# Kernel tuning notes

Measured on AMD Instinct MI355X. Metric: run time of the kernel, lower is better.

The kernel has to match this reference:

```python
import jax, jax.numpy as jnp
import numpy as np

B, CIN, COUT, H, W, DC = 16, 256, 256, 64, 64, 3


def _i2s_mask():
    # MaskedConv2d type 'B', 1x1 kernel: keep (out,in) where in-group <= out-group (mod data_channels)
    oc = np.arange(COUT) % DC
    ic = np.arange(CIN) % DC
    return jnp.asarray((ic[None, :] <= oc[:, None]).astype(np.float32))


def setup_inputs() -> dict:
    key = jax.random.key(0)
    ks = jax.random.split(key, 9)
    s = 0.05
    return {
        "x": jax.random.normal(ks[0], (B, CIN, H, W), jnp.float32),
        "w_i2s": jax.random.normal(ks[1], (COUT, CIN), jnp.float32) * s,
        "b_i2s": jax.random.normal(ks[2], (COUT,), jnp.float32) * s,
        "w_ih": jax.random.normal(ks[3], (4 * COUT, COUT), jnp.float32) * s,
        "b_ih": jax.random.normal(ks[4], (4 * COUT,), jnp.float32) * s,
        "b_hh": jax.random.normal(ks[5], (4 * COUT,), jnp.float32) * s,
        "k0": jax.random.normal(ks[6], (COUT, COUT), jnp.float32) * s,
        "k1": jax.random.normal(ks[7], (COUT, COUT), jnp.float32) * s,
        "b_s2s": jax.random.normal(ks[8], (COUT,), jnp.float32) * s,
    }


def _shift(x):
    # skew: row i shifted right by i -> [b, c, h, 2w-1]
    b, c, h, w = x.shape
    rows = jnp.arange(h)[:, None]
    cols = rows + jnp.arange(w)[None, :]
    out = jnp.zeros((b, c, h, 2 * w - 1), x.dtype)
    return out.at[:, :, rows, cols].set(x)


def _unshift(x, w):
    h = x.shape[2]
    rows = jnp.arange(h)[:, None]
    cols = rows + jnp.arange(w)[None, :]
    return x[:, :, rows, cols]  # [b, c, h, w]


def _diag_lstm(x, w_i2s, b_i2s, w_ih, b_ih, b_hh, k0, k1, b_s2s):
    b, _, h, w = x.shape
    wd = 2 * w - 1
    # masked 1x1 input-to-state conv on the skewed map
    xs = jnp.einsum('oc,bchw->bohw', w_i2s * _i2s_mask(), _shift(x)) + b_i2s[None, :, None, None]
    # per-step inputs: [wd, b*h, cout], rows flattened in (batch, height) order
    xs = xs.transpose(3, 0, 2, 1).reshape(wd, b * h, COUT)
    bias = b_ih + b_hh  # h0 is zeroed every step in the original, so W_hh never contributes

    def step(carry, x_t):
        h_prev, c = carry
        # state-to-state Conv2d k=(2,1), padding='same' (right-pad only) along flattened b*h axis
        h_next = jnp.concatenate([h_prev[1:], jnp.zeros((1, COUT), x_t.dtype)], axis=0)
        s2s = h_prev @ k0.T + h_next @ k1.T + b_s2s
        gates = (x_t + s2s) @ w_ih.T + bias
        i, f, g, o = jnp.split(gates, 4, axis=-1)
        c = jax.nn.sigmoid(f) * c + jax.nn.sigmoid(i) * jnp.tanh(g)
        h_new = jax.nn.sigmoid(o) * jnp.tanh(c)
        return (h_new, c), h_new

    z = jnp.zeros((b * h, COUT), x.dtype)
    _, hs = jax.lax.scan(step, (z, z), xs)
    # faithful to original raw .view(b, cout, h, 1): plain reshape, NOT a transpose
    outs = hs.reshape(wd, b, COUT, h).transpose(1, 2, 3, 0)  # [b, cout, h, wd]
    return _unshift(outs, w)


def reference(x, w_i2s, b_i2s, w_ih, b_ih, b_hh, k0, k1, b_s2s):
    params = (w_i2s, b_i2s, w_ih, b_ih, b_hh, k0, k1, b_s2s)
    left = _diag_lstm(x, *params)
    right = jnp.flip(_diag_lstm(jnp.flip(x, 3), *params), 3)
    right = jnp.concatenate(
        [jnp.zeros_like(right[:, :, :1, :]), right[:, :, :-1, :]], axis=2)
    return left + right
```

## Files before the change

kernel.cpp:

```cpp
#include <hip/hip_runtime.h>
#include <cstdint>
#include <cstddef>

#define BB_ 16
#define HH_ 64
#define WW_ 64
#define CC_ 256
#define WD_ 127
#define RPD 1024
#define RT_ 2048
#define NBLK 256

typedef float  f32x4 __attribute__((ext_vector_type(4)));
typedef short  s16x8 __attribute__((ext_vector_type(8)));
typedef int    i32x4 __attribute__((ext_vector_type(4)));

__device__ __forceinline__ unsigned short f2bf(float f) {
  unsigned u = __float_as_uint(f);
  u += 0x7fffu + ((u >> 16) & 1u);
  return (unsigned short)(u >> 16);
}
__device__ __forceinline__ float bf2f(unsigned short h) {
  return __uint_as_float(((unsigned)h) << 16);
}

__global__ __launch_bounds__(256) void prep_kernel(
    const float* __restrict__ w_i2s, const float* __restrict__ b_i2s,
    const float* __restrict__ w_ih,  const float* __restrict__ b_ih,
    const float* __restrict__ b_hh,  const float* __restrict__ b_s2s,
    float* __restrict__ wm, unsigned short* __restrict__ XP,
    float* __restrict__ cvec, float* __restrict__ gbias,
    unsigned* __restrict__ cnt) {
  int idx = blockIdx.x * 256 + threadIdx.x;
  if (idx < 65536) {
    int c = idx >> 8, ci = idx & 255;
    wm[idx] = ((ci % 3) <= (c % 3)) ? w_i2s[idx] : 0.0f;
  }
  int i3 = idx - 65536;
  if (i3 >= 0 && i3 < 262144) {
    int n = i3 >> 8, k = i3 & 255;
    int chb = n >> 6, g = (n >> 4) & 3, cl = n & 15;
    int j = g * 256 + chb * 16 + cl;
    float val = w_ih[j * 256 + k];
    int ks = k >> 5, l4k = (k >> 3) & 3, e = k & 7;
    size_t o = (size_t)chb * 16384 + (size_t)(ks * 4 + g) * 512 +
               (size_t)(l4k * 16 + cl) * 8 + e;
    XP[o] = f2bf(val);
  }
  int i4 = idx - 327680;
  if (i4 >= 0 && i4 < 256) cvec[i4] = b_i2s[i4] + b_s2s[i4];
  int i5 = idx - 327936;
  if (i5 >= 0 && i5 < 1024) {
    int chb = i5 >> 6, g = (i5 >> 4) & 3, cl = i5 & 15;
    int j = g * 256 + chb * 16 + cl;
    gbias[i5] = b_ih[j] + b_hh[j];
  }
  int i6 = idx - 328960;
  if (i6 >= 0 && i6 < 256) cnt[i6 * 16] = 0u;
}

__global__ __launch_bounds__(256) void prep2_kernel(
    const float* __restrict__ w_ih, const float* __restrict__ k0,
    const float* __restrict__ k1,   const float* __restrict__ cvec,
    const float* __restrict__ gbias, unsigned short* __restrict__ RP,
    float* __restrict__ gbias2) {
  __shared__ float wr[4][256];
  __shared__ float red[256];
  int bid = blockIdx.x, tid = threadIdx.x;
#pragma unroll
  for (int q = 0; q < 4; q++) {
    int n = bid * 4 + q;
    int chb = n >> 6, g = (n >> 4) & 3, cl = n & 15;
    int j = g * 256 + chb * 16 + cl;
    wr[q][tid] = w_ih[j * 256 + tid];
  }
  __syncthreads();
  int c = tid;
  float a0[4] = {0.f, 0.f, 0.f, 0.f}, a1[4] = {0.f, 0.f, 0.f, 0.f};
  for (int k = 0; k < 256; k++) {
    float v0 = k0[k * 256 + c], v1 = k1[k * 256 + c];
#pragma unroll
    for (int q = 0; q < 4; q++) {
      a0[q] = fmaf(wr[q][k], v0, a0[q]);
      a1[q] = fmaf(wr[q][k], v1, a1[q]);
    }
  }
  int ks0 = c >> 5, l40 = (c >> 3) & 3, e0 = c & 7;
#pragma unroll
  for (int q = 0; q < 4; q++) {
    int n = bid * 4 + q;
    int vv = n >> 6, nii = (n >> 4) & 3, ll = n & 15;
    size_t i0 = (size_t)vv * 32768 + (size_t)(ks0 * 4 + nii) * 512 +
                (size_t)(l40 * 16 + ll) * 8 + e0;
    size_t i1 = (size_t)vv * 32768 + (size_t)((ks0 + 8) * 4 + nii) * 512 +
                (size_t)(l40 * 16 + ll) * 8 + e0;
    RP[i0] = f2bf(a0[q]);
    RP[i1] = f2bf(a1[q]);
  }
  float cv = cvec[c];
#pragma unroll
  for (int q = 0; q < 4; q++) {
    red[tid] = wr[q][tid] * cv;
    __syncthreads();
    for (int s = 128; s > 0; s >>= 1) {
      if (tid < s) red[tid] += red[tid + s];
      __syncthreads();
    }
    if (tid == 0) { int n = bid * 4 + q; gbias2[n] = gbias[n] + red[0]; }
    __syncthreads();
  }
}

__global__ __launch_bounds__(256) void xs_kernel(
    const float* __restrict__ x, const float* __restrict__ wm,
    unsigned short* __restrict__ xs) {
  extern __shared__ float xt[];
  int blk = blockIdx.x;
  int bb = blk >> 6, ii = blk & 63;
  int tid = threadIdx.x;
  {
    const float4* src = (const float4*)(x + (((size_t)bb * 256 + tid) * 64 + ii) * 64);
    float4* dst = (float4*)(xt + tid * 64);
#pragma unroll
    for (int q = 0; q < 16; q++) dst[q] = src[q];
  }
  __syncthreads();

  int cp = tid & 127, c0 = cp * 2;
  int j0 = (tid >> 7) * 32;
  float acc0[32], acc1[32];
#pragma unroll
  for (int q = 0; q < 32; q++) { acc0[q] = 0.f; acc1[q] = 0.f; }

  for (int c4 = 0; c4 < 64; c4++) {
    float4 wa = *(const float4*)(wm + c0 * 256 + c4 * 4);
    float4 wb = *(const float4*)(wm + (c0 + 1) * 256 + c4 * 4);
    float wav[4] = {wa.x, wa.y, wa.z, wa.w};
    float wbv[4] = {wb.x, wb.y, wb.z, wb.w};
#pragma unroll
    for (int j4 = 0; j4 < 8; j4++) {
#pragma unroll
      for (int i = 0; i < 4; i++) {
        float4 xv = *(const float4*)(xt + (c4 * 4 + i) * 64 + j0 + j4 * 4);
        acc0[j4 * 4 + 0] = fmaf(wav[i], xv.x, acc0[j4 * 4 + 0]);
        acc0[j4 * 4 + 1] = fmaf(wav[i], xv.y, acc0[j4 * 4 + 1]);
        acc0[j4 * 4 + 2] = fmaf(wav[i], xv.z, acc0[j4 * 4 + 2]);
        acc0[j4 * 4 + 3] = fmaf(wav[i], xv.w, acc0[j4 * 4 + 3]);
        acc1[j4 * 4 + 0] = fmaf(wbv[i], xv.x, acc1[j4 * 4 + 0]);
        acc1[j4 * 4 + 1] = fmaf(wbv[i], xv.y, acc1[j4 * 4 + 1]);
        acc1[j4 * 4 + 2] = fmaf(wbv[i], xv.z, acc1[j4 * 4 + 2]);
        acc1[j4 * 4 + 3] = fmaf(wbv[i], xv.w, acc1[j4 * 4 + 3]);
      }
    }
  }
  size_t row = (size_t)blk;
#pragma unroll
  for (int q = 0; q < 32; q++) {
    int j = j0 + q;
    unsigned pv = (unsigned)f2bf(acc0[q]) | ((unsigned)f2bf(acc1[q]) << 16);
    *(unsigned*)(xs + ((row * 64 + j) * 256 + c0)) = pv;
    *(unsigned*)(xs + (16777216u + (row * 64 + (63 - j)) * 256 + c0)) = pv;
  }
}

__global__ __launch_bounds__(512, 2) void loop_kernel(
    const unsigned short* __restrict__ xs,
    const unsigned short* __restrict__ RP,
    const unsigned short* __restrict__ XP,
    const float* __restrict__ gbias2,
    unsigned short* __restrict__ hs,
    unsigned* __restrict__ cnt) {
  __shared__ __align__(16) unsigned short stg[16640];
  __shared__ __align__(16) unsigned short xb[32768];
  __shared__ __align__(16) float redbuf[10240];

  int bid = blockIdx.x;
  int v = bid >> 5;
  int s = (bid & 7) * 4 + ((bid >> 3) & 3);
  int r0 = s * 64;
  int tid = threadIdx.x, lane = tid & 63, w = tid >> 6;
  int rg = w >> 2, nh = (w >> 1) & 1, kh = w & 1;
  int l15 = lane & 15, l4 = lane >> 4;
  int chb = v * 2 + nh;
  int rbase = r0 + rg * 32;

  for (int idx = tid; idx < 4096; idx += 512) {
    int frag = idx >> 6, ln = idx & 63;
    int c2 = frag >> 5, rem = frag & 31;
    *(s16x8*)(xb + (size_t)idx * 8) =
        *(const s16x8*)(XP + (size_t)(v * 2 + c2) * 16384 + (size_t)rem * 512 +
                        (size_t)ln * 8);
  }
  s16x8 RB[8][4];
  {
    const unsigned short* RPb = RP + (size_t)chb * 32768 + (size_t)lane * 8;
#pragma unroll
    for (int ksl = 0; ksl < 8; ksl++)
#pragma unroll
      for (int ni = 0; ni < 4; ni++)
        RB[ksl][ni] =
            *(const s16x8*)(RPb + (size_t)((kh * 8 + ksl) * 4 + ni) * 512);
  }
  float gb[4];
#pragma unroll
  for (int ni = 0; ni < 4; ni++) gb[ni] = gbias2[chb * 64 + ni * 16 + l15];
  int ch = chb * 16 + l15;
  float cst[4] = {0.f, 0.f, 0.f, 0.f};

  int Rl0 = rbase + l15, Rl1 = Rl0 + 16;
  const unsigned short* xg0 =
      xs + (size_t)(Rl0 >> 10) * 16777216u + (size_t)(Rl0 & 1023) * 16384;
  const unsigned short* xg1 =
      xs + (size_t)(Rl1 >> 10) * 16777216u + (size_t)(Rl1 & 1023) * 16384;
  int ii0 = rg * 32 + l15, ii1 = ii0 + 16;
  int tlo = rg * 32, thi = rg * 32 + 94;
  bool km1 = kh && ((s & 15) == 15) && (rg == 1) && (l15 == 15);
  bool nbwave = (w == 0) && ((s & 15) != 15);
  unsigned* myc = cnt + ((s * 8 + (lane & 7)) * 16);
  unsigned* nbc = cnt + (((s + 1) * 8 + (lane & 7)) * 16);
  unsigned* pubc = cnt + ((s * 8 + v) * 16);
  int rsw = ((l15 + kh) & 7) << 4;
  int ar0b = (rg * 32 + l15 + kh) * 512;
  int ar1b = ar0b + 8192;
  const s16x8 zz = {0, 0, 0, 0, 0, 0, 0, 0};

  __syncthreads();

  for (int t = 0; t < 127; ++t) {
    f32x4 accA[4], accB[4];
#pragma unroll
    for (int ni = 0; ni < 4; ni++) {
      accA[ni] = (f32x4){0.f, 0.f, 0.f, 0.f};
      accB[ni] = (f32x4){0.f, 0.f, 0.f, 0.f};
    }
    if (t >= tlo && t <= thi) {
      int j0 = t - ii0, j1 = t - ii1;
      bool ib0 = ((unsigned)j0 < 64u), ib1 = ((unsigned)j1 < 64u);
      const unsigned short* px0 = xg0 + (ptrdiff_t)j0 * 256;
      const unsigned short* px1 = xg1 + (ptrdiff_t)j1 * 256;
#pragma unroll
      for (int ksl = 0; ksl < 4; ksl++) {
        int kk = (kh * 4 + ksl) * 32 + l4 * 8;
        s16x8 a0 = ib0 ? *(const s16x8*)(px0 + kk) : zz;
        s16x8 a1 = ib1 ? *(const s16x8*)(px1 + kk) : zz;
        const unsigned short* bb =
            xb + ((size_t)((nh * 8 + kh * 4 + ksl) * 4) * 64 + (size_t)lane) * 8;
#pragma unroll
        for (int ni = 0; ni < 4; ni++) {
          s16x8 b = *(const s16x8*)(bb + (size_t)ni * 512);
          accA[ni] = __builtin_amdgcn_mfma_f32_16x16x32_bf16(a0, b, accA[ni], 0, 0, 0);
          accB[ni] = __builtin_amdgcn_mfma_f32_16x16x32_bf16(a1, b, accB[ni], 0, 0, 0);
        }
      }
    }

    if (t > 0) {
      unsigned tgt = (unsigned)t * 8u;
      while (true) {
        unsigned c_ = __hip_atomic_load(myc, __ATOMIC_RELAXED,
                                        __HIP_MEMORY_SCOPE_AGENT);
        if (__all(c_ >= tgt)) break;
        __builtin_amdgcn_s_sleep(1);
      }
      if (nbwave) {
        while (true) {
          unsigned c_ = __hip_atomic_load(nbc, __ATOMIC_RELAXED,
                                          __HIP_MEMORY_SCOPE_AGENT);
          if (__all(c_ >= tgt)) break;
          __builtin_amdgcn_s_sleep(1);
        }
      }
      const unsigned short* src = hs + (size_t)(t - 1) * 524288 + (size_t)r0 * 256;
      i32x4 sv0, sv1, sv2, sv3, sv4;
      asm volatile("global_load_dwordx4 %0, %1, off sc0 sc1"
                   : "=v"(sv0) : "v"(src + (size_t)tid * 8));
      asm volatile("global_load_dwordx4 %0, %1, off sc0 sc1"
                   : "=v"(sv1) : "v"(src + (size_t)(tid + 512) * 8));
      asm volatile("global_load_dwordx4 %0, %1, off sc0 sc1"
                   : "=v"(sv2) : "v"(src + (size_t)(tid + 1024) * 8));
      asm volatile("global_load_dwordx4 %0, %1, off sc0 sc1"
                   : "=v"(sv3) : "v"(src + (size_t)(tid + 1536) * 8));
      if (tid < 32)
        asm volatile("global_load_dwordx4 %0, %1, off sc0 sc1"
                     : "=v"(sv4) : "v"(src + (size_t)(tid + 2048) * 8));
      asm volatile("s_waitcnt vmcnt(0)" ::: "memory");
      __builtin_amdgcn_sched_barrier(0);
      {
        int rA = tid >> 5, cA = (tid & 31) * 16;
        *(i32x4*)((char*)stg + (rA +  0) * 512 + (cA ^ (((rA +  0) & 7) << 4))) = sv0;
        *(i32x4*)((char*)stg + (rA + 16) * 512 + (cA ^ (((rA + 16) & 7) << 4))) = sv1;
        *(i32x4*)((char*)stg + (rA + 32) * 512 + (cA ^ (((rA + 32) & 7) << 4))) = sv2;
        *(i32x4*)((char*)stg + (rA + 48) * 512 + (cA ^ (((rA + 48) & 7) << 4))) = sv3;
        if (tid < 32)
          *(i32x4*)((char*)stg + 64 * 512 + (tid * 16)) = sv4;
      }
      __syncthreads();
#pragma unroll
      for (int ksl = 0; ksl < 8; ksl++) {
        int cb = ((ksl * 64 + l4 * 16) ^ rsw);
        s16x8 a0 = *(const s16x8*)((const char*)stg + ar0b + cb);
        s16x8 a1 = *(const s16x8*)((const char*)stg + ar1b + cb);
        a1 = km1 ? zz : a1;
#pragma unroll
        for (int ni = 0; ni < 4; ni++) {
          accA[ni] = __builtin_amdgcn_mfma_f32_16x16x32_bf16(a0, RB[ksl][ni], accA[ni], 0, 0, 0);
          accB[ni] = __builtin_amdgcn_mfma_f32_16x16x32_bf16(a1, RB[ksl][ni], accB[ni], 0, 0, 0);
        }
      }
    }

    {
      float* wsl = redbuf + (size_t)(((rg * 2 + nh) * 2 + (kh ^ 1)) * 1280);
#pragma unroll
      for (int ni = 0; ni < 4; ni++) {
        f32x4 wv = kh ? accA[ni] : accB[ni];
        *(f32x4*)(wsl + (size_t)((ni * 16 + l15) * 20 + l4 * 4)) = wv;
      }
    }
    __syncthreads();
    f32x4 ov[4];
    {
      const float* rsl = redbuf + (size_t)(((rg * 2 + nh) * 2 + kh) * 1280);
#pragma unroll
      for (int ni = 0; ni < 4; ni++) {
        f32x4 p = *(const f32x4*)(rsl + (size_t)((ni * 16 + l15) * 20 + l4 * 4));
        ov[ni] = (kh ? accB[ni] : accA[ni]) + p;
      }
    }
    unsigned short* hout = hs + (size_t)t * 524288;
#pragma unroll
    for (int r = 0; r < 4; r++) {
      int R = rbase + kh * 16 + l4 * 4 + r;
      float xi = ov[0][r] + gb[0];
      float xf = ov[1][r] + gb[1];
      float xg_ = ov[2][r] + gb[2];
      float xo = ov[3][r] + gb[3];
      float si = 1.f / (1.f + __expf(-xi));
      float sf = 1.f / (1.f + __expf(-xf));
      float so = 1.f / (1.f + __expf(-xo));
      float tg = 1.f - 2.f / (__expf(2.f * xg_) + 1.f);
      float cn = sf * cst[r] + si * tg;
      cst[r] = cn;
      float th = 1.f - 2.f / (__expf(2.f * cn) + 1.f);
      unsigned short hv = f2bf(so * th);
      const unsigned short* pst = hout + (size_t)R * 256 + ch;
      asm volatile("global_store_short %0, %1, off sc0 sc1"
                   :: "v"(pst), "v"(hv));
    }
    asm volatile("s_waitcnt vmcnt(0)" ::: "memory");
    __builtin_amdgcn_sched_barrier(0);
    if (lane == 0)
      __hip_atomic_fetch_add(pubc, 1u, __ATOMIC_RELAXED,
                             __HIP_MEMORY_SCOPE_AGENT);
  }
}

__global__ __launch_bounds__(256) void gather_kernel(
    const unsigned short* __restrict__ hs, float* __restrict__ out) {
  __shared__ unsigned short slab0[127 * 66 + 2];
  __shared__ unsigned short slab1[127 * 66 + 2];
  int blk = blockIdx.x;
  int bb = blk >> 8, o = blk & 255;
  int row = bb * 64 + (o >> 2);
  int c0 = (o & 3) * 64;
  int tid = threadIdx.x;
  for (int idx = tid; idx < 127 * 32; idx += 256) {
    int tt = idx >> 5, cu = idx & 31;
    unsigned v0 = *(const unsigned*)(hs + ((size_t)tt * RT_ + row) * 256 + c0 + cu * 2);
    unsigned v1 = *(const unsigned*)(hs + ((size_t)tt * RT_ + 1024 + row) * 256 + c0 + cu * 2);
    *(unsigned*)(slab0 + tt * 66 + cu * 2) = v0;
    *(unsigned*)(slab1 + tt * 66 + cu * 2) = v1;
  }
  __syncthreads();
  int j = tid & 63;
  int hh0 = (tid >> 6) * 16;
  float* ob = out + (size_t)blk * 4096;
  for (int hh = hh0; hh < hh0 + 16; hh++) {
    float v = bf2f(slab0[(hh + j) * 66 + hh]);
    if (hh > 0) v += bf2f(slab1[(hh - 1 + 63 - j) * 66 + (hh - 1)]);
    ob[hh * 64 + j] = v;
  }
}

extern "C" void kernel_launch(void* const* d_in, const int* in_sizes, int n_in,
                              void* d_out, int out_size, void* d_ws, size_t ws_size,
                              hipStream_t stream) {
  const float* x     = (const float*)d_in[0];
  const float* w_i2s = (const float*)d_in[1];
  const float* b_i2s = (const float*)d_in[2];
  const float* w_ih  = (const float*)d_in[3];
  const float* b_ih  = (const float*)d_in[4];
  const float* b_hh  = (const float*)d_in[5];
  const float* k0    = (const float*)d_in[6];
  const float* k1    = (const float*)d_in[7];
  const float* b_s2s = (const float*)d_in[8];
  float* out = (float*)d_out;

  char* ws = (char*)d_ws;
  float*          wm     = (float*)(ws + 0);
  float*          cvec   = (float*)(ws + 262144);
  float*          gbias  = (float*)(ws + 263168);
  float*          gbias2 = (float*)(ws + 267264);
  unsigned*       cnt    = (unsigned*)(ws + 271360);
  unsigned short* XP     = (unsigned short*)(ws + 287744);
  unsigned short* RP     = (unsigned short*)(ws + 812032);
  unsigned short* xs     = (unsigned short*)(ws + 1860608);
  unsigned short* hs     = (unsigned short*)(ws + 68969472);
  const size_t NEEDED = 202138624;
  if (ws_size < NEEDED) return;

  prep_kernel<<<1286, 256, 0, stream>>>(w_i2s, b_i2s, w_ih, b_ih, b_hh, b_s2s,
                                        wm, XP, cvec, gbias, cnt);
  prep2_kernel<<<256, 256, 0, stream>>>(w_ih, k0, k1, cvec, gbias, RP, gbias2);
  xs_kernel<<<1024, 256, 65536, stream>>>(x, wm, xs);

  {
    const unsigned short* a0 = xs;
    const unsigned short* a1 = RP;
    const unsigned short* a2 = XP;
    const float*          a3 = gbias2;
    unsigned short*       a4 = hs;
    unsigned*             a5 = cnt;
    void* kargs[6] = {(void*)&a0, (void*)&a1, (void*)&a2,
                      (void*)&a3, (void*)&a4, (void*)&a5};
    hipLaunchCooperativeKernel((const void*)loop_kernel, dim3(NBLK), dim3(512),
                               kargs, 0, stream);
  }

  gather_kernel<<<4096, 256, 0, stream>>>(hs, out);
}
```

Baseline: 1.131 ms.

## Prefetch next-step input GEMM and replace counters with per-block step tags

The input-projection MFMAs for step t+1 now run after the gate update of step t, ahead of the inter-block wait, so they overlap synchronization latency. Per-wave atomic counters are replaced by per-block monotonically increasing tags written once after a block barrier, with one wave polling them. Staging of the previous hidden state switches to direct global-to-LDS loads with a swizzled layout, and MFMA priority is raised during the recurrent GEMM. This adds block-wide barriers per step and changes the visibility ordering of the sync protocol, so any race would corrupt results.

```diff
diff --git a/kernel.cpp b/kernel.cpp
--- a/kernel.cpp
+++ b/kernel.cpp
@@ -24,13 +24,20 @@
   return __uint_as_float(((unsigned)h) << 16);
 }
 
+__device__ __forceinline__ void gl_lds16(const unsigned short* g,
+                                         unsigned short* l) {
+  __builtin_amdgcn_global_load_lds(
+      (const __attribute__((address_space(1))) void*)g,
+      (__attribute__((address_space(3))) void*)l, 16, 0, 0);
+}
+
 __global__ __launch_bounds__(256) void prep_kernel(
     const float* __restrict__ w_i2s, const float* __restrict__ b_i2s,
     const float* __restrict__ w_ih,  const float* __restrict__ b_ih,
     const float* __restrict__ b_hh,  const float* __restrict__ b_s2s,
     float* __restrict__ wm, unsigned short* __restrict__ XP,
     float* __restrict__ cvec, float* __restrict__ gbias,
-    unsigned* __restrict__ cnt) {
+    unsigned* __restrict__ tags) {
   int idx = blockIdx.x * 256 + threadIdx.x;
   if (idx < 65536) {
     int c = idx >> 8, ci = idx & 255;
@@ -56,7 +63,7 @@
     gbias[i5] = b_ih[j] + b_hh[j];
   }
   int i6 = idx - 328960;
-  if (i6 >= 0 && i6 < 256) cnt[i6 * 16] = 0u;
+  if (i6 >= 0 && i6 < 512) tags[i6] = 0u;
 }
 
 __global__ __launch_bounds__(256) void prep2_kernel(
@@ -169,8 +176,8 @@
     const unsigned short* __restrict__ XP,
     const float* __restrict__ gbias2,
     unsigned short* __restrict__ hs,
-    unsigned* __restrict__ cnt) {
-  __shared__ __align__(16) unsigned short stg[16640];
+    unsigned* __restrict__ tags) {
+  __shared__ __align__(16) unsigned short stg[16896];
   __shared__ __align__(16) unsigned short xb[32768];
   __shared__ __align__(16) float redbuf[10240];
 
@@ -215,24 +222,34 @@
   int ii0 = rg * 32 + l15, ii1 = ii0 + 16;
   int tlo = rg * 32, thi = rg * 32 + 94;
   bool km1 = kh && ((s & 15) == 15) && (rg == 1) && (l15 == 15);
-  bool nbwave = (w == 0) && ((s & 15) != 15);
-  unsigned* myc = cnt + ((s * 8 + (lane & 7)) * 16);
-  unsigned* nbc = cnt + (((s + 1) * 8 + (lane & 7)) * 16);
-  unsigned* pubc = cnt + ((s * 8 + v) * 16);
+  bool neednb = ((s & 15) != 15);
+  int pls = (lane < 8) ? s : (neednb ? (s + 1) : s);
+  const unsigned* ptT = tags + pls * 16 + (lane & 7);
+  bool pactive = (lane < 8) || ((lane < 16) && neednb);
+  unsigned* stT = tags + s * 16 + v;
   int rsw = ((l15 + kh) & 7) << 4;
   int ar0b = (rg * 32 + l15 + kh) * 512;
   int ar1b = ar0b + 8192;
+  int c5 = lane & 31, l5 = lane >> 5;
+  int soff[4];
+#pragma unroll
+  for (int m = 0; m < 4; m++) {
+    int row = 2 * m + l5;
+    int csrc = (c5 & 24) | ((c5 ^ row) & 7);
+    soff[m] = row * 256 + csrc * 8;
+  }
   const s16x8 zz = {0, 0, 0, 0, 0, 0, 0, 0};
 
   __syncthreads();
 
-  for (int t = 0; t < 127; ++t) {
-    f32x4 accA[4], accB[4];
-#pragma unroll
-    for (int ni = 0; ni < 4; ni++) {
-      accA[ni] = (f32x4){0.f, 0.f, 0.f, 0.f};
-      accB[ni] = (f32x4){0.f, 0.f, 0.f, 0.f};
-    }
+  f32x4 accA[4], accB[4];
+#pragma unroll
+  for (int ni = 0; ni < 4; ni++) {
+    accA[ni] = (f32x4){0.f, 0.f, 0.f, 0.f};
+    accB[ni] = (f32x4){0.f, 0.f, 0.f, 0.f};
+  }
+  {
+    int t = 0;
     if (t >= tlo && t <= thi) {
       int j0 = t - ii0, j1 = t - ii1;
       bool ib0 = ((unsigned)j0 < 64u), ib1 = ((unsigned)j1 < 64u);
@@ -253,48 +270,34 @@
         }
       }
     }
-
+  }
+
+  for (int t = 0; t < 127; ++t) {
     if (t > 0) {
-      unsigned tgt = (unsigned)t * 8u;
-      while (true) {
-        unsigned c_ = __hip_atomic_load(myc, __ATOMIC_RELAXED,
-                                        __HIP_MEMORY_SCOPE_AGENT);
-        if (__all(c_ >= tgt)) break;
-        __builtin_amdgcn_s_sleep(1);
-      }
-      if (nbwave) {
+      if (w == 0) {
+        unsigned tgt = (unsigned)t;
         while (true) {
-          unsigned c_ = __hip_atomic_load(nbc, __ATOMIC_RELAXED,
-                                          __HIP_MEMORY_SCOPE_AGENT);
-          if (__all(c_ >= tgt)) break;
+          unsigned tv;
+          asm volatile("global_load_dword %0, %1, off sc0 sc1"
+                       : "=v"(tv) : "v"(ptT));
+          asm volatile("s_waitcnt vmcnt(0)" ::: "memory");
+          if (__all(!pactive || (tv >= tgt))) break;
           __builtin_amdgcn_s_sleep(1);
         }
       }
-      const unsigned short* src = hs + (size_t)(t - 1) * 524288 + (size_t)r0 * 256;
-      i32x4 sv0, sv1, sv2, sv3, sv4;
-      asm volatile("global_load_dwordx4 %0, %1, off sc0 sc1"
-                   : "=v"(sv0) : "v"(src + (size_t)tid * 8));
-      asm volatile("global_load_dwordx4 %0, %1, off sc0 sc1"
-                   : "=v"(sv1) : "v"(src + (size_t)(tid + 512) * 8));
-      asm volatile("global_load_dwordx4 %0, %1, off sc0 sc1"
-                   : "=v"(sv2) : "v"(src + (size_t)(tid + 1024) * 8));
-      asm volatile("global_load_dwordx4 %0, %1, off sc0 sc1"
-                   : "=v"(sv3) : "v"(src + (size_t)(tid + 1536) * 8));
-      if (tid < 32)
-        asm volatile("global_load_dwordx4 %0, %1, off sc0 sc1"
-                     : "=v"(sv4) : "v"(src + (size_t)(tid + 2048) * 8));
+      __syncthreads();
+      const unsigned short* src =
+          hs + (size_t)(t - 1) * 524288 + (size_t)r0 * 256;
+      const unsigned short* pw = src + w * 2048;
+      gl_lds16(pw + soff[0], stg + (w * 4 + 0) * 512);
+      gl_lds16(pw + soff[1], stg + (w * 4 + 1) * 512);
+      gl_lds16(pw + soff[2], stg + (w * 4 + 2) * 512);
+      gl_lds16(pw + soff[3], stg + (w * 4 + 3) * 512);
+      if (w == 0) gl_lds16(src + 16384 + soff[0], stg + 32 * 512);
       asm volatile("s_waitcnt vmcnt(0)" ::: "memory");
       __builtin_amdgcn_sched_barrier(0);
-      {
-        int rA = tid >> 5, cA = (tid & 31) * 16;
-        *(i32x4*)((char*)stg + (rA +  0) * 512 + (cA ^ (((rA +  0) & 7) << 4))) = sv0;
-        *(i32x4*)((char*)stg + (rA + 16) * 512 + (cA ^ (((rA + 16) & 7) << 4))) = sv1;
-        *(i32x4*)((char*)stg + (rA + 32) * 512 + (cA ^ (((rA + 32) & 7) << 4))) = sv2;
-        *(i32x4*)((char*)stg + (rA + 48) * 512 + (cA ^ (((rA + 48) & 7) << 4))) = sv3;
-        if (tid < 32)
-          *(i32x4*)((char*)stg + 64 * 512 + (tid * 16)) = sv4;
-      }
       __syncthreads();
+      __builtin_amdgcn_s_setprio(1);
 #pragma unroll
       for (int ksl = 0; ksl < 8; ksl++) {
         int cb = ((ksl * 64 + l4 * 16) ^ rsw);
@@ -307,6 +310,7 @@
           accB[ni] = __builtin_amdgcn_mfma_f32_16x16x32_bf16(a1, RB[ksl][ni], accB[ni], 0, 0, 0);
         }
       }
+      __builtin_amdgcn_s_setprio(0);
     }
 
     {
@@ -347,11 +351,41 @@
       asm volatile("global_store_short %0, %1, off sc0 sc1"
                    :: "v"(pst), "v"(hv));
     }
+#pragma unroll
+    for (int ni = 0; ni < 4; ni++) {
+      accA[ni] = (f32x4){0.f, 0.f, 0.f, 0.f};
+      accB[ni] = (f32x4){0.f, 0.f, 0.f, 0.f};
+    }
+    if (t < 126) {
+      int tn = t + 1;
+      if (tn >= tlo && tn <= thi) {
+        int j0 = tn - ii0, j1 = tn - ii1;
+        bool ib0 = ((unsigned)j0 < 64u), ib1 = ((unsigned)j1 < 64u);
+        const unsigned short* px0 = xg0 + (ptrdiff_t)j0 * 256;
+        const unsigned short* px1 = xg1 + (ptrdiff_t)j1 * 256;
+#pragma unroll
+        for (int ksl = 0; ksl < 4; ksl++) {
+          int kk = (kh * 4 + ksl) * 32 + l4 * 8;
+          s16x8 a0 = ib0 ? *(const s16x8*)(px0 + kk) : zz;
+          s16x8 a1 = ib1 ? *(const s16x8*)(px1 + kk) : zz;
+          const unsigned short* bb =
+              xb + ((size_t)((nh * 8 + kh * 4 + ksl) * 4) * 64 + (size_t)lane) * 8;
+#pragma unroll
+          for (int ni = 0; ni < 4; ni++) {
+            s16x8 b = *(const s16x8*)(bb + (size_t)ni * 512);
+            accA[ni] = __builtin_amdgcn_mfma_f32_16x16x32_bf16(a0, b, accA[ni], 0, 0, 0);
+            accB[ni] = __builtin_amdgcn_mfma_f32_16x16x32_bf16(a1, b, accB[ni], 0, 0, 0);
+          }
+        }
+      }
+    }
     asm volatile("s_waitcnt vmcnt(0)" ::: "memory");
-    __builtin_amdgcn_sched_barrier(0);
-    if (lane == 0)
-      __hip_atomic_fetch_add(pubc, 1u, __ATOMIC_RELAXED,
-                             __HIP_MEMORY_SCOPE_AGENT);
+    __syncthreads();
+    if (tid == 0 && t < 126) {
+      unsigned tv = (unsigned)(t + 1);
+      asm volatile("global_store_dword %0, %1, off sc0 sc1"
+                   :: "v"(stT), "v"(tv));
+    }
   }
 }
 
@@ -401,7 +435,7 @@
   float*          cvec   = (float*)(ws + 262144);
   float*          gbias  = (float*)(ws + 263168);
   float*          gbias2 = (float*)(ws + 267264);
-  unsigned*       cnt    = (unsigned*)(ws + 271360);
+  unsigned*       tags   = (unsigned*)(ws + 271360);
   unsigned short* XP     = (unsigned short*)(ws + 287744);
   unsigned short* RP     = (unsigned short*)(ws + 812032);
   unsigned short* xs     = (unsigned short*)(ws + 1860608);
@@ -410,7 +444,7 @@
   if (ws_size < NEEDED) return;
 
   prep_kernel<<<1286, 256, 0, stream>>>(w_i2s, b_i2s, w_ih, b_ih, b_hh, b_s2s,
-                                        wm, XP, cvec, gbias, cnt);
+                                        wm, XP, cvec, gbias, tags);
   prep2_kernel<<<256, 256, 0, stream>>>(w_ih, k0, k1, cvec, gbias, RP, gbias2);
   xs_kernel<<<1024, 256, 65536, stream>>>(x, wm, xs);
 
@@ -420,7 +454,7 @@
     const unsigned short* a2 = XP;
     const float*          a3 = gbias2;
     unsigned short*       a4 = hs;
-    unsigned*             a5 = cnt;
+    unsigned*             a5 = tags;
     void* kargs[6] = {(void*)&a0, (void*)&a1, (void*)&a2,
                       (void*)&a3, (void*)&a4, (void*)&a5};
     hipLaunchCooperativeKernel((const void*)loop_kernel, dim3(NBLK), dim3(512),
```

Result: faster. 1.086 ms (-4.0%).
